# Kernel optimization log

Measured on AMD Instinct MI355X. Metric: run time of the kernel, lower is better.

The kernel has to match this reference:

```python
import jax, jax.numpy as jnp
import numpy as np

N_NODES = 10000
N_EDGES = 160000
D = 256
P = 2.0  # exponent in |h_i - h_j|**p


def setup_inputs() -> dict:
    key = jax.random.key(0)
    k1, k2, k3, k4 = jax.random.split(key, 4)
    X = jax.random.normal(k1, (N_NODES, D), dtype=jnp.float32)
    edge_index = jax.random.randint(k2, (2, N_EDGES), 0, N_NODES, dtype=jnp.int64)
    # SAGEConv parameters (scaled like Glorot init)
    scale = 1.0 / np.sqrt(D)
    W_root = jax.random.normal(k3, (D, D), dtype=jnp.float32) * scale
    W_neigh = jax.random.normal(k4, (D, D), dtype=jnp.float32) * scale
    b = jnp.zeros((D,), dtype=jnp.float32)
    return {"X": X, "edge_index": edge_index, "W_root": W_root,
            "W_neigh": W_neigh, "b": b}


def reference(X, edge_index, W_root, W_neigh, b):
    n = X.shape[0]
    row, col = edge_index[0], edge_index[1]
    # degree of each target (row) node, used for both SAGE mean and scatter-mean
    ones = jnp.ones((row.shape[0],), dtype=X.dtype)
    deg = jax.ops.segment_sum(ones, row, num_segments=n)           # [N]
    denom = jnp.maximum(deg, 1.0)[:, None]                         # avoid 0-div
    # SAGEConv: h_i = W_root x_i + W_neigh mean_{j in N(i)} x_j + b
    neigh_sum = jax.ops.segment_sum(X[col], row, num_segments=n)   # [N, D]
    neigh_mean = neigh_sum / denom
    H = jax.nn.relu(X @ W_root + neigh_mean @ W_neigh + b)         # [N, D]
    # gather node diffs -> pow -> scatter-mean by row -> tanh
    diffs = jnp.abs(H[row] - H[col]) ** P                          # [E, D]
    gg = jax.ops.segment_sum(diffs, row, num_segments=n) / denom   # [N, D]
    return jnp.tanh(gg)
```

## Files before the change

### kernel.cpp

```cpp
#include <hip/hip_runtime.h>
#include <math.h>

#define N_NODES 10000
#define N_EDGES 160000
#define D 256
#define KDIM 512
#define CAP 64
#define SPLIT 5000

typedef short bf16x8 __attribute__((ext_vector_type(8)));
typedef float f32x4 __attribute__((ext_vector_type(4)));
typedef unsigned short ushort_t;

__device__ __forceinline__ ushort_t f2bf(float f) {
    unsigned u = __builtin_bit_cast(unsigned, f);
    unsigned r = (u + 0x7fffu + ((u >> 16) & 1u)) >> 16;
    return (ushort_t)r;
}
__device__ __forceinline__ float bf2f(ushort_t u) {
    unsigned v = ((unsigned)u) << 16;
    return __builtin_bit_cast(float, v);
}

#define ZERO_BLOCKS 79
#define PREPW_BLOCKS 128
#define CASTX_BLOCKS 2500

__global__ void k_init(int* __restrict__ cursors,
                       const float* __restrict__ Wr, const float* __restrict__ Wn,
                       ushort_t* __restrict__ Wb,
                       const float* __restrict__ X, ushort_t* __restrict__ A) {
    __shared__ float tile[32][33];
    int b = blockIdx.x;
    int t = threadIdx.x;
    if (b < ZERO_BLOCKS) {
        int i = b * 256 + t;
        if (i < 2 * N_NODES) cursors[i] = 0;
    } else if (b < ZERO_BLOCKS + PREPW_BLOCKS) {
        int wb = b - ZERO_BLOCKS;
        int k0 = (wb & 15) * 32, n0 = (wb >> 4) * 32;
        {
            int r = t >> 3, c4 = t & 7;
            int k = k0 + r;
            const float* src = (k < D) ? (Wr + (size_t)k * D + n0 + c4 * 4)
                                       : (Wn + (size_t)(k - D) * D + n0 + c4 * 4);
            float4 v = *(const float4*)src;
            tile[r][c4 * 4 + 0] = v.x; tile[r][c4 * 4 + 1] = v.y;
            tile[r][c4 * 4 + 2] = v.z; tile[r][c4 * 4 + 3] = v.w;
        }
        __syncthreads();
        {
            int n = t >> 3, kq = t & 7;
            ushort4 o = make_ushort4(f2bf(tile[kq * 4 + 0][n]), f2bf(tile[kq * 4 + 1][n]),
                                     f2bf(tile[kq * 4 + 2][n]), f2bf(tile[kq * 4 + 3][n]));
            *(ushort4*)(Wb + (size_t)(n0 + n) * KDIM + k0 + kq * 4) = o;
        }
    } else {
        int nb = b - ZERO_BLOCKS - PREPW_BLOCKS;
        int node = nb * 4 + (t >> 6), lane = t & 63;
        if (node < N_NODES) {
            float4 v = *(const float4*)(X + (size_t)node * D + lane * 4);
            ushort4 o = make_ushort4(f2bf(v.x), f2bf(v.y), f2bf(v.z), f2bf(v.w));
            *(ushort4*)(A + (size_t)node * KDIM + lane * 4) = o;
        }
    }
}

__global__ void k_fill(const int* __restrict__ row, const int* __restrict__ col,
                       int* __restrict__ curLo, int* __restrict__ curHi,
                       int* __restrict__ csr_col, int e) {
    int i = blockIdx.x * blockDim.x + threadIdx.x;
    if (i < e) {
        int r = row[i], c = col[i];
        if (c < SPLIT) {
            int p = atomicAdd(&curLo[r], 1);
            csr_col[r * CAP + p] = c;
        } else {
            int p = atomicAdd(&curHi[r], 1);
            csr_col[r * CAP + CAP - 1 - p] = c;
        }
    }
}

__global__ void k_mean(const int* __restrict__ curLo, const int* __restrict__ curHi,
                       const int* __restrict__ csr_col, ushort_t* __restrict__ A) {
    int node = blockIdx.x * 4 + (threadIdx.x >> 6);
    int lane = threadIdx.x & 63;
    if (node >= N_NODES) return;
    int s0 = node * CAP;
    int nlo = curLo[node], nhi = curHi[node];
    float ax = 0.f, ay = 0.f, az = 0.f, aw = 0.f;
    #pragma unroll 1
    for (int half = 0; half < 2; ++half) {
        int s = half ? (s0 + CAP - nhi) : s0;
        int t = half ? (s0 + CAP) : (s0 + nlo);
        int e = s;
        for (; e + 4 <= t; e += 4) {
            int j0 = csr_col[e], j1 = csr_col[e + 1], j2 = csr_col[e + 2], j3 = csr_col[e + 3];
            ushort4 v0 = *(const ushort4*)(A + (size_t)j0 * KDIM + lane * 4);
            ushort4 v1 = *(const ushort4*)(A + (size_t)j1 * KDIM + lane * 4);
            ushort4 v2 = *(const ushort4*)(A + (size_t)j2 * KDIM + lane * 4);
            ushort4 v3 = *(const ushort4*)(A + (size_t)j3 * KDIM + lane * 4);
            ax += bf2f(v0.x) + bf2f(v1.x) + bf2f(v2.x) + bf2f(v3.x);
            ay += bf2f(v0.y) + bf2f(v1.y) + bf2f(v2.y) + bf2f(v3.y);
            az += bf2f(v0.z) + bf2f(v1.z) + bf2f(v2.z) + bf2f(v3.z);
            aw += bf2f(v0.w) + bf2f(v1.w) + bf2f(v2.w) + bf2f(v3.w);
        }
        for (; e < t; ++e) {
            int j = csr_col[e];
            ushort4 v = *(const ushort4*)(A + (size_t)j * KDIM + lane * 4);
            ax += bf2f(v.x); ay += bf2f(v.y); az += bf2f(v.z); aw += bf2f(v.w);
        }
    }
    int deg = nlo + nhi;
    float inv = 1.f / (float)(deg > 1 ? deg : 1);
    ushort4 o = make_ushort4(f2bf(ax * inv), f2bf(ay * inv), f2bf(az * inv), f2bf(aw * inv));
    *(ushort4*)(A + (size_t)node * KDIM + D + lane * 4) = o;
}

#define BM 64
#define BN 128
#define BK 32
#define LDK 40

__global__ __launch_bounds__(256) void k_gemm(
    const ushort_t* __restrict__ A, const ushort_t* __restrict__ Wb,
    const float* __restrict__ bias, ushort_t* __restrict__ H) {
    __shared__ ushort_t As[BM][LDK];
    __shared__ ushort_t Bs[BN][LDK];

    int tid = threadIdx.x;
    int lane = tid & 63;
    int wave = tid >> 6;
    int wm = wave >> 1;
    int wn = wave & 1;
    int row0 = blockIdx.x * BM;
    int col0 = blockIdx.y * BN;

    f32x4 acc[2][4];
    #pragma unroll
    for (int i = 0; i < 2; ++i)
        #pragma unroll
        for (int j = 0; j < 4; ++j)
            acc[i][j] = (f32x4){0.f, 0.f, 0.f, 0.f};

    int r_a = tid >> 2;
    int kq = tid & 3;

    for (int kk = 0; kk < KDIM; kk += BK) {
        int ga = row0 + r_a; if (ga >= N_NODES) ga = N_NODES - 1;
        ushort4 a0 = *(const ushort4*)(A + (size_t)ga * KDIM + kk + kq * 8);
        ushort4 a1 = *(const ushort4*)(A + (size_t)ga * KDIM + kk + kq * 8 + 4);
        ushort4 b0 = *(const ushort4*)(Wb + (size_t)(col0 + r_a) * KDIM + kk + kq * 8);
        ushort4 b1 = *(const ushort4*)(Wb + (size_t)(col0 + r_a) * KDIM + kk + kq * 8 + 4);
        ushort4 b2 = *(const ushort4*)(Wb + (size_t)(col0 + r_a + 64) * KDIM + kk + kq * 8);
        ushort4 b3 = *(const ushort4*)(Wb + (size_t)(col0 + r_a + 64) * KDIM + kk + kq * 8 + 4);

        __syncthreads();
        *(ushort4*)&As[r_a][kq * 8]          = a0;
        *(ushort4*)&As[r_a][kq * 8 + 4]      = a1;
        *(ushort4*)&Bs[r_a][kq * 8]          = b0;
        *(ushort4*)&Bs[r_a][kq * 8 + 4]      = b1;
        *(ushort4*)&Bs[r_a + 64][kq * 8]     = b2;
        *(ushort4*)&Bs[r_a + 64][kq * 8 + 4] = b3;
        __syncthreads();

        int fr = lane & 15, fg = (lane >> 4) * 8;
        bf16x8 aF[2], bF[4];
        #pragma unroll
        for (int mf = 0; mf < 2; ++mf)
            aF[mf] = *(const bf16x8*)&As[wm * 32 + mf * 16 + fr][fg];
        #pragma unroll
        for (int nf = 0; nf < 4; ++nf)
            bF[nf] = *(const bf16x8*)&Bs[wn * 64 + nf * 16 + fr][fg];
        #pragma unroll
        for (int mf = 0; mf < 2; ++mf)
            #pragma unroll
            for (int nf = 0; nf < 4; ++nf)
                acc[mf][nf] = __builtin_amdgcn_mfma_f32_16x16x32_bf16(
                    aF[mf], bF[nf], acc[mf][nf], 0, 0, 0);
    }

    int fc = lane & 15, frow = (lane >> 4) * 4;
    #pragma unroll
    for (int nf = 0; nf < 4; ++nf) {
        int c = col0 + wn * 64 + nf * 16 + fc;
        float bc = bias[c];
        #pragma unroll
        for (int mf = 0; mf < 2; ++mf) {
            #pragma unroll
            for (int q = 0; q < 4; ++q) {
                int r = row0 + wm * 32 + mf * 16 + frow + q;
                if (r < N_NODES) {
                    float h = acc[mf][nf][q] + bc;
                    H[(size_t)r * D + c] = f2bf(h > 0.f ? h : 0.f);
                }
            }
        }
    }
}

__global__ void k_out(const ushort_t* __restrict__ H,
                      const int* __restrict__ curLo, const int* __restrict__ curHi,
                      const int* __restrict__ csr_col,
                      float* __restrict__ out) {
    int node = blockIdx.x * 4 + (threadIdx.x >> 6);
    int lane = threadIdx.x & 63;
    if (node >= N_NODES) return;
    ushort4 hb = *(const ushort4*)(H + (size_t)node * D + lane * 4);
    float hx = bf2f(hb.x), hy = bf2f(hb.y), hz = bf2f(hb.z), hw = bf2f(hb.w);
    int s0 = node * CAP;
    int nlo = curLo[node], nhi = curHi[node];
    float ax = 0.f, ay = 0.f, az = 0.f, aw = 0.f;
    #pragma unroll 1
    for (int half = 0; half < 2; ++half) {
        int s = half ? (s0 + CAP - nhi) : s0;
        int t = half ? (s0 + CAP) : (s0 + nlo);
        int e = s;
        for (; e + 4 <= t; e += 4) {
            int j0 = csr_col[e], j1 = csr_col[e + 1], j2 = csr_col[e + 2], j3 = csr_col[e + 3];
            ushort4 v0 = *(const ushort4*)(H + (size_t)j0 * D + lane * 4);
            ushort4 v1 = *(const ushort4*)(H + (size_t)j1 * D + lane * 4);
            ushort4 v2 = *(const ushort4*)(H + (size_t)j2 * D + lane * 4);
            ushort4 v3 = *(const ushort4*)(H + (size_t)j3 * D + lane * 4);
            float d;
            d = hx - bf2f(v0.x); ax += d * d;  d = hy - bf2f(v0.y); ay += d * d;
            d = hz - bf2f(v0.z); az += d * d;  d = hw - bf2f(v0.w); aw += d * d;
            d = hx - bf2f(v1.x); ax += d * d;  d = hy - bf2f(v1.y); ay += d * d;
            d = hz - bf2f(v1.z); az += d * d;  d = hw - bf2f(v1.w); aw += d * d;
            d = hx - bf2f(v2.x); ax += d * d;  d = hy - bf2f(v2.y); ay += d * d;
            d = hz - bf2f(v2.z); az += d * d;  d = hw - bf2f(v2.w); aw += d * d;
            d = hx - bf2f(v3.x); ax += d * d;  d = hy - bf2f(v3.y); ay += d * d;
            d = hz - bf2f(v3.z); az += d * d;  d = hw - bf2f(v3.w); aw += d * d;
        }
        for (; e < t; ++e) {
            int j = csr_col[e];
            ushort4 v = *(const ushort4*)(H + (size_t)j * D + lane * 4);
            float d;
            d = hx - bf2f(v.x); ax += d * d;  d = hy - bf2f(v.y); ay += d * d;
            d = hz - bf2f(v.z); az += d * d;  d = hw - bf2f(v.w); aw += d * d;
        }
    }
    int deg = nlo + nhi;
    float inv = 1.f / (float)(deg > 1 ? deg : 1);
    float4 o;
    o.x = tanhf(ax * inv); o.y = tanhf(ay * inv);
    o.z = tanhf(az * inv); o.w = tanhf(aw * inv);
    *(float4*)(out + (size_t)node * D + lane * 4) = o;
}


extern "C" void kernel_launch(void* const* d_in, const int* in_sizes, int n_in,
                              void* d_out, int out_size, void* d_ws, size_t ws_size,
                              hipStream_t stream) {
    const float* X    = (const float*)d_in[0];
    const int*   edge = (const int*)d_in[1];
    const float* Wr   = (const float*)d_in[2];
    const float* Wn   = (const float*)d_in[3];
    const float* bias = (const float*)d_in[4];
    float* out = (float*)d_out;

    char* ws = (char*)d_ws;
    size_t off = 0;
    auto alloc = [&](size_t bytes) -> void* {
        void* p = ws + off;
        off += (bytes + 255) & ~(size_t)255;
        return p;
    };
    int*      cursors = (int*)alloc(sizeof(int) * 2 * N_NODES);
    int*      csr_col = (int*)alloc(sizeof(int) * N_NODES * CAP);
    ushort_t* A       = (ushort_t*)alloc(sizeof(ushort_t) * (size_t)N_NODES * KDIM);
    ushort_t* Wb      = (ushort_t*)alloc(sizeof(ushort_t) * (size_t)D * KDIM);
    ushort_t* H       = (ushort_t*)alloc(sizeof(ushort_t) * (size_t)N_NODES * D);

    int* curLo = cursors;
    int* curHi = cursors + N_NODES;
    const int* row = edge;
    const int* col = edge + N_EDGES;

    k_init<<<ZERO_BLOCKS + PREPW_BLOCKS + CASTX_BLOCKS, 256, 0, stream>>>(
        cursors, Wr, Wn, Wb, X, A);
    k_fill<<<(N_EDGES + 255) / 256, 256, 0, stream>>>(row, col, curLo, curHi,
                                                      csr_col, N_EDGES);
    k_mean<<<2500, 256, 0, stream>>>(curLo, curHi, csr_col, A);

    dim3 ggrid((N_NODES + BM - 1) / BM, D / BN);
    k_gemm<<<ggrid, 256, 0, stream>>>(A, Wb, bias, H);

    k_out<<<2500, 256, 0, stream>>>(H, curLo, curHi, csr_col, out);
}
```

Measured before the change: 65.60 us.

## Fuse CSR fill into init kernel with in-kernel grid barrier

Merges the cursor-zeroing and edge bucket-fill kernels into the init kernel, so that one launch is removed. A spin-wait barrier on a global counter separates zeroing from the atomic fills. It also switches the final output write to a nontemporal store. The barrier assumes all 625 fill blocks are co-resident, and it is placed ahead of the other block types in the same grid, which risks deadlock or extra stall time. The counters are reset by the last block.

After: 249.1 us. +279.8%, slower.

```diff
diff --git a/kernel.cpp b/kernel.cpp
--- a/kernel.cpp
+++ b/kernel.cpp
@@ -22,22 +22,56 @@
     return __builtin_bit_cast(float, v);
 }
 
-#define ZERO_BLOCKS 79
+__device__ int g_c1 = 0;
+__device__ int g_c2 = 0;
+
+#define FILL_BLOCKS 625
 #define PREPW_BLOCKS 128
 #define CASTX_BLOCKS 2500
 
-__global__ void k_init(int* __restrict__ cursors,
+__global__ void k_init(const int* __restrict__ row, const int* __restrict__ col,
+                       int* __restrict__ cursors ,
+                       int* __restrict__ csr_col,
                        const float* __restrict__ Wr, const float* __restrict__ Wn,
                        ushort_t* __restrict__ Wb,
                        const float* __restrict__ X, ushort_t* __restrict__ A) {
     __shared__ float tile[32][33];
     int b = blockIdx.x;
     int t = threadIdx.x;
-    if (b < ZERO_BLOCKS) {
+    if (b < FILL_BLOCKS) {
+        int base = b * 32;
+        if (t < 32 && base + t < 2 * N_NODES) cursors[base + t] = 0;
+        __threadfence();
+        __syncthreads();
+        if (t == 0) {
+            atomicAdd(&g_c1, 1);
+            while (atomicAdd(&g_c1, 0) < FILL_BLOCKS) { }
+        }
+        __syncthreads();
+        __threadfence();
         int i = b * 256 + t;
-        if (i < 2 * N_NODES) cursors[i] = 0;
-    } else if (b < ZERO_BLOCKS + PREPW_BLOCKS) {
-        int wb = b - ZERO_BLOCKS;
+        if (i < N_EDGES) {
+            int r = row[i], c = col[i];
+            if (c < SPLIT) {
+                int p = atomicAdd(&cursors[r], 1);
+                csr_col[r * CAP + p] = c;
+            } else {
+                int p = atomicAdd(&cursors[N_NODES + r], 1);
+                csr_col[r * CAP + CAP - 1 - p] = c;
+            }
+        }
+        __threadfence();
+        __syncthreads();
+        if (t == 0) {
+            int prev = atomicAdd(&g_c2, 1);
+            if (prev == FILL_BLOCKS - 1) {
+                g_c2 = 0;
+                g_c1 = 0;
+                __threadfence();
+            }
+        }
+    } else if (b < FILL_BLOCKS + PREPW_BLOCKS) {
+        int wb = b - FILL_BLOCKS;
         int k0 = (wb & 15) * 32, n0 = (wb >> 4) * 32;
         {
             int r = t >> 3, c4 = t & 7;
@@ -56,28 +90,12 @@
             *(ushort4*)(Wb + (size_t)(n0 + n) * KDIM + k0 + kq * 4) = o;
         }
     } else {
-        int nb = b - ZERO_BLOCKS - PREPW_BLOCKS;
+        int nb = b - FILL_BLOCKS - PREPW_BLOCKS;
         int node = nb * 4 + (t >> 6), lane = t & 63;
         if (node < N_NODES) {
             float4 v = *(const float4*)(X + (size_t)node * D + lane * 4);
             ushort4 o = make_ushort4(f2bf(v.x), f2bf(v.y), f2bf(v.z), f2bf(v.w));
             *(ushort4*)(A + (size_t)node * KDIM + lane * 4) = o;
-        }
-    }
-}
-
-__global__ void k_fill(const int* __restrict__ row, const int* __restrict__ col,
-                       int* __restrict__ curLo, int* __restrict__ curHi,
-                       int* __restrict__ csr_col, int e) {
-    int i = blockIdx.x * blockDim.x + threadIdx.x;
-    if (i < e) {
-        int r = row[i], c = col[i];
-        if (c < SPLIT) {
-            int p = atomicAdd(&curLo[r], 1);
-            csr_col[r * CAP + p] = c;
-        } else {
-            int p = atomicAdd(&curHi[r], 1);
-            csr_col[r * CAP + CAP - 1 - p] = c;
         }
     }
 }
@@ -243,10 +261,10 @@
     }
     int deg = nlo + nhi;
     float inv = 1.f / (float)(deg > 1 ? deg : 1);
-    float4 o;
-    o.x = tanhf(ax * inv); o.y = tanhf(ay * inv);
-    o.z = tanhf(az * inv); o.w = tanhf(aw * inv);
-    *(float4*)(out + (size_t)node * D + lane * 4) = o;
+    f32x4 o;
+    o[0] = tanhf(ax * inv); o[1] = tanhf(ay * inv);
+    o[2] = tanhf(az * inv); o[3] = tanhf(aw * inv);
+    __builtin_nontemporal_store(o, (f32x4*)(out + (size_t)node * D + lane * 4));
 }
 
 
@@ -278,10 +296,8 @@
     const int* row = edge;
     const int* col = edge + N_EDGES;
 
-    k_init<<<ZERO_BLOCKS + PREPW_BLOCKS + CASTX_BLOCKS, 256, 0, stream>>>(
-        cursors, Wr, Wn, Wb, X, A);
-    k_fill<<<(N_EDGES + 255) / 256, 256, 0, stream>>>(row, col, curLo, curHi,
-                                                      csr_col, N_EDGES);
+    k_init<<<FILL_BLOCKS + PREPW_BLOCKS + CASTX_BLOCKS, 256, 0, stream>>>(
+        row, col, cursors, csr_col, Wr, Wn, Wb, X, A);
     k_mean<<<2500, 256, 0, stream>>>(curLo, curHi, csr_col, A);
 
     dim3 ggrid((N_NODES + BM - 1) / BM, D / BN);
```
